# Kernel optimization log

Hardware: AMD Instinct MI355X
Metric: run time of the kernel (lower is better)

The kernel has to match this reference:

```python
import jax, jax.numpy as jnp
import numpy as np

B, CIN, COUT, H, W = 4, 256, 256, 64, 64
EPS = 1e-5


def _conv1x1(x, w, b):
    # x: [B,C,H,W], w: [O,C], b: [O]
    return jnp.einsum('bchw,oc->bohw', x, w) + b[:, None, None]


def _conv3x3(x, w, b):
    y = jax.lax.conv_general_dilated(x, w, (1, 1), 'SAME',
                                     dimension_numbers=('NCHW', 'OIHW', 'NCHW'))
    return y + b[:, None, None]


def _bn(x, g, b, m, v):
    # inference-mode BatchNorm2d
    return g[:, None, None] * (x - m[:, None, None]) * jax.lax.rsqrt(v[:, None, None] + EPS) + b[:, None, None]


def setup_inputs():
    key = jax.random.key(0)
    keys = iter(jax.random.split(key, 64))
    nrm = lambda shape, s=0.05: jax.random.normal(next(keys), shape, dtype=jnp.float32) * s
    uni = lambda shape: jax.random.uniform(next(keys), shape, dtype=jnp.float32, minval=0.5, maxval=1.5)
    C, C2 = COUT, COUT // 2
    d = {}
    d['x'] = nrm((B, CIN, H, W), 1.0)
    d['wq'] = nrm((C2, CIN)); d['bq'] = nrm((C2,))
    d['wk'] = nrm((C2, CIN)); d['bk'] = nrm((C2,))
    d['wv'] = nrm((C, CIN)); d['bv'] = nrm((C,))
    d['d1_w'] = nrm((C, C)); d['d1_b'] = nrm((C,))
    for p in ['bn1', 'lbn1', 'lbn2', 'lbn3']:
        d[p + '_g'] = uni((C,)); d[p + '_b'] = nrm((C,))
        d[p + '_m'] = nrm((C,)); d[p + '_v'] = uni((C,))
    d['l1_w'] = nrm((C, C)); d['l1_b'] = nrm((C,))
    d['l2_w'] = nrm((C, C, 3, 3)); d['l2_b'] = nrm((C,))
    d['l3_w'] = nrm((C, C)); d['l3_b'] = nrm((C,))
    d['r1_w'] = nrm((C2, C)); d['r1_b'] = nrm((C2,))
    d['rbn_g'] = uni((C2,)); d['rbn_b'] = nrm((C2,))
    d['rbn_m'] = nrm((C2,)); d['rbn_v'] = uni((C2,))
    d['r2_w'] = nrm((C, C2)); d['r2_b'] = nrm((C,))
    return d


def _forward(x, wq, bq, wk, bk, wv, bv, d1_w, d1_b,
             bn1_g, bn1_b, bn1_m, bn1_v,
             l1_w, l1_b, lbn1_g, lbn1_b, lbn1_m, lbn1_v,
             l2_w, l2_b, lbn2_g, lbn2_b, lbn2_m, lbn2_v,
             l3_w, l3_b, lbn3_g, lbn3_b, lbn3_m, lbn3_v,
             r1_w, r1_b, rbn_g, rbn_b, rbn_m, rbn_v, r2_w, r2_b):
    b, _, h, w = x.shape
    n = h * w
    q = _conv1x1(x, wq, bq).reshape(b, -1, n)   # [B, C/2, N]
    k = _conv1x1(x, wk, bk).reshape(b, -1, n)   # [B, C/2, N]
    v = _conv1x1(x, wv, bv).reshape(b, -1, n)   # [B, C,   N]
    energy = jnp.einsum('bcn,bcm->bnm', q, k)   # [B, N, N] (query^T key)
    attn = jax.nn.softmax(energy, axis=-1)
    # feature = bmm(value, attn^T): feat[b,c,n] = sum_m v[b,c,m] * attn[b,n,m]
    feat = jnp.einsum('bcm,bnm->bcn', v, attn).reshape(b, -1, h, w)
    # dual1 gate: sigmoid(relu(bn(conv1x1(feat))))
    gate1 = jax.nn.sigmoid(jax.nn.relu(_bn(_conv1x1(feat, d1_w, d1_b), bn1_g, bn1_b, bn1_m, bn1_v)))
    y = feat * gate1
    # dual2_l: 1x1 -> 3x3 -> 1x1 conv/bn/relu stack
    yl = jax.nn.relu(_bn(_conv1x1(y, l1_w, l1_b), lbn1_g, lbn1_b, lbn1_m, lbn1_v))
    yl = jax.nn.relu(_bn(_conv3x3(yl, l2_w, l2_b), lbn2_g, lbn2_b, lbn2_m, lbn2_v))
    yl = jax.nn.relu(_bn(_conv1x1(yl, l3_w, l3_b), lbn3_g, lbn3_b, lbn3_m, lbn3_v))
    # dual2_r: global-avg-pool SE branch
    pooled = jnp.mean(y, axis=(2, 3), keepdims=True)  # [B, C, 1, 1]
    yr = jax.nn.relu(_bn(_conv1x1(pooled, r1_w, r1_b), rbn_g, rbn_b, rbn_m, rbn_v))
    yr = _conv1x1(yr, r2_w, r2_b)
    return feat * jax.nn.sigmoid(yl + yr)


def reference(x, wq, bq, wk, bk, wv, bv, d1_w, d1_b,
              bn1_g, bn1_b, bn1_m, bn1_v,
              l1_w, l1_b, lbn1_g, lbn1_b, lbn1_m, lbn1_v,
              l2_w, l2_b, lbn2_g, lbn2_b, lbn2_m, lbn2_v,
              l3_w, l3_b, lbn3_g, lbn3_b, lbn3_m, lbn3_v,
              r1_w, r1_b, rbn_g, rbn_b, rbn_m, rbn_v, r2_w, r2_b):
    return _forward(x, wq, bq, wk, bk, wv, bv, d1_w, d1_b,
                    bn1_g, bn1_b, bn1_m, bn1_v,
                    l1_w, l1_b, lbn1_g, lbn1_b, lbn1_m, lbn1_v,
                    l2_w, l2_b, lbn2_g, lbn2_b, lbn2_m, lbn2_v,
                    l3_w, l3_b, lbn3_g, lbn3_b, lbn3_m, lbn3_v,
                    r1_w, r1_b, rbn_g, rbn_b, rbn_m, rbn_v, r2_w, r2_b)
```

## Files before the change

kernel.cpp:

```cpp
#include <hip/hip_runtime.h>
#include <math.h>

#define NPIX 4096
#define EPSBN 1e-5f

typedef __attribute__((ext_vector_type(8))) short bf16x8;
typedef __attribute__((ext_vector_type(4))) float f32x4;

__device__ __forceinline__ float sigmoidf_(float x) { return 1.0f / (1.0f + expf(-x)); }

__device__ __forceinline__ short f2bf(float f) {
    unsigned u = __float_as_uint(f);
    u += 0x7fffu + ((u >> 16) & 1u);
    return (short)(u >> 16);
}
__device__ __forceinline__ float bf2f(short s) {
    return __uint_as_float(((unsigned)(unsigned short)s) << 16);
}
__device__ __forceinline__ int pk2(float lo, float hi) {
    return (int)(unsigned short)f2bf(lo) | ((int)(unsigned short)f2bf(hi) << 16);
}

__device__ __forceinline__ void gl_lds16(const short* g, short* l) {
    __builtin_amdgcn_global_load_lds(
        (const __attribute__((address_space(1))) void*)g,
        (__attribute__((address_space(3))) void*)l, 16, 0, 0);
}

template <int EPI, int BM, int BN>
__global__ __launch_bounds__(256) void gbt_k(
    const short* __restrict__ A, int lda,
    const short* __restrict__ B, int ldb,
    void* __restrict__ Cv, void* __restrict__ Cv2, int Ktot,
    const float* __restrict__ bias, const float* __restrict__ bias2,
    const float* __restrict__ bng, const float* __restrict__ bnb,
    const float* __restrict__ bnm, const float* __restrict__ bnv,
    const short* __restrict__ aux, const float* __restrict__ yrp)
{
    constexpr int FI = BM / 32, FJ = BN / 32;
    constexpr int SA = BM / 64, SB = BN / 64;
    __shared__ alignas(16) short lsA[2 * BM * 32];
    __shared__ alignas(16) short lsB[2 * BN * 32];

    const int tid = threadIdx.x;
    const int l = tid & 63;
    const int wv = tid >> 6;
    const int wm = wv >> 1, wn = wv & 1;
    const int m0 = blockIdx.y * BM;
    const int n0 = blockIdx.x * BN;

    const short* arow[2];
    const short* brow[2];
#pragma unroll
    for (int s = 0; s < SA; ++s) {
        int r = wv * (16 * SA) + s * 16 + (l >> 2);
        int sd = (l & 3) ^ ((r >> 1) & 3);
        if (EPI == 5) {
            int g = m0 + r;
            int p = (g >> 12) * 4356 + (((g & 4095) >> 6) + 1) * 66 + ((g & 63) + 1);
            arow[s] = A + (size_t)p * 256 + (sd << 3);
        } else {
            arow[s] = A + (size_t)(m0 + r) * lda + (sd << 3);
        }
    }
#pragma unroll
    for (int s = 0; s < SB; ++s) {
        int r = wv * (16 * SB) + s * 16 + (l >> 2);
        int sd = (l & 3) ^ ((r >> 1) & 3);
        brow[s] = B + (size_t)(n0 + r) * ldb + (sd << 3);
    }

    const int ks = l >> 4;
    const int lc = l & 15;
    int aoff[FI], boff[FJ];
#pragma unroll
    for (int f = 0; f < FI; ++f) {
        int ra = wm * (BM / 2) + f * 16 + lc;
        aoff[f] = ra * 64 + ((ks ^ ((ra >> 1) & 3)) << 4);
    }
#pragma unroll
    for (int f = 0; f < FJ; ++f) {
        int rb = wn * (BN / 2) + f * 16 + lc;
        boff[f] = rb * 64 + ((ks ^ ((rb >> 1) & 3)) << 4);
    }

    auto stage = [&](int d, int k0l) {
        int eA, eB;
        if (EPI == 5) {
            int t = k0l >> 8, ci0 = k0l & 255;
            eA = ((t / 3) * 66 + (t % 3) - 67) * 256 + ci0;
            eB = t * 65536 + ci0;
        } else {
            eA = k0l; eB = k0l;
        }
        short* dA = lsA + d * (BM * 32) + wv * (SA * 512);
        short* dB = lsB + d * (BN * 32) + wv * (SB * 512);
#pragma unroll
        for (int s = 0; s < SA; ++s) gl_lds16(arow[s] + eA, dA + s * 512);
#pragma unroll
        for (int s = 0; s < SB; ++s) gl_lds16(brow[s] + eB, dB + s * 512);
    };

    f32x4 acc[FI][FJ] = {};
    const int nt = Ktot >> 5;

    stage(0, 0);
    __syncthreads();
    int cur = 0;
    for (int t = 0; t < nt; ++t) {
        if (t + 1 < nt) stage(cur ^ 1, (t + 1) << 5);
        bf16x8 af[FI], bfr[FJ];
#pragma unroll
        for (int f = 0; f < FI; ++f)
            af[f] = *(const bf16x8*)((const char*)lsA + cur * (BM * 64) + aoff[f]);
#pragma unroll
        for (int f = 0; f < FJ; ++f)
            bfr[f] = *(const bf16x8*)((const char*)lsB + cur * (BN * 64) + boff[f]);
#pragma unroll
        for (int i = 0; i < FI; ++i)
#pragma unroll
            for (int j = 0; j < FJ; ++j)
                acc[i][j] = __builtin_amdgcn_mfma_f32_16x16x32_bf16(af[i], bfr[j], acc[i][j], 0, 0, 0);
        __syncthreads();
        cur ^= 1;
    }

    const int lr = (l >> 4) << 2;
#pragma unroll
    for (int i = 0; i < FI; ++i) {
        const int rowl = wm * (BM / 2) + i * 16 + lr;
#pragma unroll
        for (int j = 0; j < FJ; ++j) {
            const int coll = n0 + wn * (BN / 2) + j * 16 + lc;

            float sc = 0.f, tc = 0.f, bi = 0.f;
            if constexpr (EPI == 1) {
                bi = (coll < 128) ? bias[coll] : bias2[coll - 128];
            } else if constexpr (EPI == 3 || EPI == 4 || EPI == 5) {
                sc = bng[coll] * rsqrtf(bnv[coll] + EPSBN);
                tc = bnb[coll] - bnm[coll] * sc;
                bi = bias[coll];
            }

#pragma unroll
            for (int r = 0; r < 4; ++r) {
                const int row = m0 + rowl + r;
                float vvv = acc[i][j][r];
                if constexpr (EPI == 1) {
                    float val = vvv + bi;
                    short hi = f2bf(val);
                    short lo = f2bf(val - bf2f(hi));
                    size_t rb = (size_t)row * 256;
                    if (coll < 128) {
                        short* qb_ = (short*)Cv;
                        qb_[rb + coll] = hi;
                        qb_[rb + 128 + coll] = lo;
                    } else {
                        short* kb_ = (short*)Cv2;
                        int c = coll - 128;
                        kb_[rb + c] = hi;
                        kb_[rb + 128 + c] = lo;
                    }
                } else if constexpr (EPI == 2) {
                    int bb = coll >> 12;
                    ((short*)Cv)[((size_t)bb * 256 + row) * 4096 + (coll & 4095)] = f2bf(vvv + bias[row]);
                } else if constexpr (EPI == 3) {
                    float g = sigmoidf_(fmaxf(sc * (vvv + bi) + tc, 0.f));
                    float fv = bf2f(aux[(size_t)row * 256 + coll]);
                    ((short*)Cv)[(size_t)row * 256 + coll] = f2bf(fv * g);
                } else if constexpr (EPI == 4) {
                    float rv = fmaxf(sc * (vvv + bi) + tc, 0.f);
                    int bb = row >> 12, n = row & 4095;
                    int pr = bb * 4356 + ((n >> 6) + 1) * 66 + (n & 63) + 1;
                    ((short*)Cv)[(size_t)pr * 256 + coll] = f2bf(rv);
                } else if constexpr (EPI == 5) {
                    float rv = fmaxf(sc * (vvv + bi) + tc, 0.f);
                    ((short*)Cv)[(size_t)row * 256 + coll] = f2bf(rv);
                } else if constexpr (EPI == 6) {
                    float s6 = bng[row] * rsqrtf(bnv[row] + EPSBN);
                    float t6 = bnb[row] - bnm[row] * s6;
                    int bb = coll >> 12;
                    float yl = fmaxf(s6 * (vvv + bias[row]) + t6, 0.f);
                    float sg = sigmoidf_(yl + yrp[bb * 256 + row]);
                    float fv = bf2f(aux[(size_t)coll * 256 + row]);
                    ((float*)Cv)[((size_t)bb * 256 + row) * 4096 + (coll & 4095)] = fv * sg;
                }
            }
        }
    }
}

__global__ __launch_bounds__(512, 2) void flash_k(
    const short* __restrict__ Q, const short* __restrict__ K,
    const short* __restrict__ V, float* __restrict__ Op, float* __restrict__ lp)
{
    __shared__ alignas(16) short smem[32768];

    const int tid = threadIdx.x;
    const int l = tid & 63;
    const int wv = tid >> 6;
    const int bid = blockIdx.x;
    const int combo = bid & 15;
    const int batch = combo >> 2;
    const int kvq = combo & 3;
    const int q0 = (bid >> 4) * 256;
    const int kv0 = kvq * 1024;

    const short* Qb = Q + (size_t)batch * 4096 * 256;
    const short* Kb = K + (size_t)batch * 4096 * 256;
    const short* Vb = V + (size_t)batch * 256 * 4096;

    const int lc = l & 15, ks = l >> 4;

    bf16x8 bq[2][8];
#pragma unroll
    for (int f = 0; f < 2; ++f)
#pragma unroll
        for (int cc = 0; cc < 8; ++cc)
            bq[f][cc] = *(const bf16x8*)(Qb +
                (size_t)(q0 + wv * 32 + f * 16 + lc) * 256 + cc * 32 + ks * 8);

    const short* ksrc[2]; short* kdst[2];
    const short* vsrc[2]; short* vdst[2];
#pragma unroll
    for (int i = 0; i < 2; ++i) {
        int row = wv * 4 + i * 2 + (l >> 5);
        int s = l & 31;
        int g = s ^ (row & 7);
        ksrc[i] = Kb + (size_t)(kv0 + row) * 256 + g * 8;
        kdst[i] = smem + wv * 1024 + i * 512;
        int c = wv * 32 + i * 16 + (l >> 2);
        int sv = l & 3;
        int gv = sv ^ ((c >> 1) & 3);
        vsrc[i] = Vb + (size_t)c * 4096 + kv0 + gv * 8;
        vdst[i] = smem + 16384 + wv * 1024 + i * 512;
    }
    auto stageKV = [&](int buf, int t) {
#pragma unroll
        for (int i = 0; i < 2; ++i) gl_lds16(ksrc[i] + (size_t)t * 8192, kdst[i] + buf * 8192);
#pragma unroll
        for (int i = 0; i < 2; ++i) gl_lds16(vsrc[i] + t * 32, vdst[i] + buf * 8192);
    };

    stageKV(0, 0);
    __syncthreads();

    const int kro = lc * 512;
    const int kxr = lc & 7;
    const int vb0 = lc * 64 + ((ks ^ ((lc >> 1) & 3)) << 4);
    const int addrA = (((ks & 1) * 2) * 16 + lc) * 4;
    const int addrB = addrA + 64;

    bf16x8 ones;
#pragma unroll
    for (int e = 0; e < 8; ++e) ones[e] = (short)0x3F80;

    f32x4 acc_o[2][16] = {};
    f32x4 acc_l[2] = {};

    int cur = 0;
    for (int t = 0; t < 32; ++t) {
        if (t + 1 < 32) stageKV(cur ^ 1, t + 1);

        const char* kb_ = (const char*)smem + cur * 16384;
        f32x4 s00 = {}, s01 = {}, s10 = {}, s11 = {};
        __builtin_amdgcn_s_setprio(1);
#pragma unroll
        for (int jc = 0; jc < 4; ++jc) {
#pragma unroll
            for (int kvf = 0; kvf < 2; ++kvf) {
                const char* rb_ = kb_ + kro + kvf * 8192;
                bf16x8 kh_ = *(const bf16x8*)(rb_ + ((((jc * 4) + ks) ^ kxr) << 4));
                bf16x8 kl_ = *(const bf16x8*)(rb_ + (((((jc + 4) * 4) + ks) ^ kxr) << 4));
                f32x4& sA = kvf ? s01 : s00;
                f32x4& sB = kvf ? s11 : s10;
                sA = __builtin_amdgcn_mfma_f32_16x16x32_bf16(kh_, bq[0][jc], sA, 0, 0, 0);
                sB = __builtin_amdgcn_mfma_f32_16x16x32_bf16(kh_, bq[1][jc], sB, 0, 0, 0);
                sA = __builtin_amdgcn_mfma_f32_16x16x32_bf16(kl_, bq[0][jc], sA, 0, 0, 0);
                sB = __builtin_amdgcn_mfma_f32_16x16x32_bf16(kl_, bq[1][jc], sB, 0, 0, 0);
                sA = __builtin_amdgcn_mfma_f32_16x16x32_bf16(kh_, bq[0][jc + 4], sA, 0, 0, 0);
                sB = __builtin_amdgcn_mfma_f32_16x16x32_bf16(kh_, bq[1][jc + 4], sB, 0, 0, 0);
            }
        }
        __builtin_amdgcn_s_setprio(0);

        bf16x8 pa[2];
#pragma unroll
        for (int f = 0; f < 2; ++f) {
            const f32x4& sa = f ? s10 : s00;
            const f32x4& sb = f ? s11 : s01;
            int u0 = pk2(__expf(sa[0]), __expf(sa[1]));
            int u1 = pk2(__expf(sa[2]), __expf(sa[3]));
            int u2 = pk2(__expf(sb[0]), __expf(sb[1]));
            int u3 = pk2(__expf(sb[2]), __expf(sb[3]));
            int a0 = __builtin_amdgcn_ds_bpermute(addrA, u0);
            int b0 = __builtin_amdgcn_ds_bpermute(addrA, u2);
            int a1 = __builtin_amdgcn_ds_bpermute(addrA, u1);
            int b1 = __builtin_amdgcn_ds_bpermute(addrA, u3);
            int a2 = __builtin_amdgcn_ds_bpermute(addrB, u0);
            int b2 = __builtin_amdgcn_ds_bpermute(addrB, u2);
            int a3 = __builtin_amdgcn_ds_bpermute(addrB, u1);
            int b3 = __builtin_amdgcn_ds_bpermute(addrB, u3);
            union { int i4[4]; bf16x8 v; } un;
            un.i4[0] = (ks < 2) ? a0 : b0;
            un.i4[1] = (ks < 2) ? a1 : b1;
            un.i4[2] = (ks < 2) ? a2 : b2;
            un.i4[3] = (ks < 2) ? a3 : b3;
            pa[f] = un.v;
        }

        const char* vbb = (const char*)smem + 32768 + cur * 16384;
        __builtin_amdgcn_s_setprio(1);
#pragma unroll
        for (int j = 0; j < 16; ++j) {
            bf16x8 vv = *(const bf16x8*)(vbb + vb0 + j * 1024);
            acc_o[0][j] = __builtin_amdgcn_mfma_f32_16x16x32_bf16(pa[0], vv, acc_o[0][j], 0, 0, 0);
            acc_o[1][j] = __builtin_amdgcn_mfma_f32_16x16x32_bf16(pa[1], vv, acc_o[1][j], 0, 0, 0);
        }
        acc_l[0] = __builtin_amdgcn_mfma_f32_16x16x32_bf16(pa[0], ones, acc_l[0], 0, 0, 0);
        acc_l[1] = __builtin_amdgcn_mfma_f32_16x16x32_bf16(pa[1], ones, acc_l[1], 0, 0, 0);
        __builtin_amdgcn_s_setprio(0);
        __syncthreads();
        cur ^= 1;
    }

    float* Ob = Op + ((size_t)combo * 4096 + q0 + wv * 32) * 256;
#pragma unroll
    for (int f = 0; f < 2; ++f)
#pragma unroll
        for (int j = 0; j < 16; ++j)
#pragma unroll
            for (int r = 0; r < 4; ++r)
                Ob[(size_t)(f * 16 + ks * 4 + r) * 256 + j * 16 + lc] = acc_o[f][j][r];
    if (lc == 0) {
        float* lb = lp + (size_t)combo * 4096 + q0 + wv * 32;
#pragma unroll
        for (int f = 0; f < 2; ++f)
#pragma unroll
            for (int r = 0; r < 4; ++r)
                lb[f * 16 + ks * 4 + r] = acc_l[f][r];
    }
}

__global__ __launch_bounds__(256) void combine_k(const float* __restrict__ Op,
                                                 const float* __restrict__ lp,
                                                 short* __restrict__ o)
{
    int idx = blockIdx.x * 256 + threadIdx.x;
    size_t e = (size_t)idx * 4;
    int row = (int)(e >> 8);
    int batch = row >> 12, ql = row & 4095;
    int c = (int)(e & 255);
    size_t lbase = (size_t)batch * 4 * 4096 + ql;
    float li = 1.0f / (lp[lbase] + lp[lbase + 4096] + lp[lbase + 8192] + lp[lbase + 12288]);
    size_t base = ((size_t)(batch * 4) * 4096 + ql) * 256 + c;
    const float4 a = *(const float4*)(Op + base);
    const float4 b = *(const float4*)(Op + base + 1048576);
    const float4 cc = *(const float4*)(Op + base + 2097152);
    const float4 d = *(const float4*)(Op + base + 3145728);
    short4 o4;
    o4.x = f2bf((a.x + b.x + cc.x + d.x) * li);
    o4.y = f2bf((a.y + b.y + cc.y + d.y) * li);
    o4.z = f2bf((a.z + b.z + cc.z + d.z) * li);
    o4.w = f2bf((a.w + b.w + cc.w + d.w) * li);
    *(short4*)(o + (size_t)row * 256 + c) = o4;
}

__global__ __launch_bounds__(256) void transpose_x_k(const float* __restrict__ x,
                                                     short* __restrict__ xT3)
{
    __shared__ float t[64][65];
    const int b = blockIdx.z, c0 = blockIdx.y * 64, n0 = blockIdx.x * 64;
    const int tid = threadIdx.x;
#pragma unroll
    for (int rep = 0; rep < 16; ++rep) {
        int idx = tid + rep * 256;
        int i = idx >> 6, j = idx & 63;
        t[i][j] = x[((size_t)(b * 256 + c0 + i)) * NPIX + n0 + j];
    }
    __syncthreads();
#pragma unroll
    for (int rep = 0; rep < 16; ++rep) {
        int idx = tid + rep * 256;
        int i = idx >> 6, j = idx & 63;
        float v = t[j][i];
        short hi = f2bf(v);
        short lo = f2bf(v - bf2f(hi));
        size_t rb = ((size_t)(b * NPIX + n0 + i)) * 768;
        xT3[rb + c0 + j] = hi;
        xT3[rb + 256 + c0 + j] = hi;
        xT3[rb + 512 + c0 + j] = lo;
    }
}

__global__ __launch_bounds__(256) void cvt_hilo3_k(const float* __restrict__ src,
                                                   short* __restrict__ dst)
{
    int idx = blockIdx.x * 256 + threadIdx.x;
    int o = idx >> 8, c = idx & 255;
    float v = src[idx];
    short hi = f2bf(v);
    short lo = f2bf(v - bf2f(hi));
    size_t rb = (size_t)o * 768;
    dst[rb + c] = hi;
    dst[rb + 256 + c] = lo;
    dst[rb + 512 + c] = hi;
}

__global__ __launch_bounds__(256) void cvt_k(const float* __restrict__ s,
                                             short* __restrict__ d, int n)
{
    int i = blockIdx.x * 256 + threadIdx.x;
    if (i < n) d[i] = f2bf(s[i]);
}

__global__ __launch_bounds__(256) void permw2_k(const float* __restrict__ l2w,
                                                short* __restrict__ w2)
{
    int idx = blockIdx.x * 256 + threadIdx.x;
    int t = idx >> 16;
    int rem = idx & 65535;
    int co = rem >> 8, ci = rem & 255;
    w2[idx] = f2bf(l2w[((size_t)(co * 256 + ci)) * 9 + t]);
}

__global__ __launch_bounds__(256) void pool_s1_k(const short* __restrict__ yT,
                                                 float* __restrict__ ppart)
{
    const int ns = blockIdx.x, cg = blockIdx.y, b = blockIdx.z;
    const int tid = threadIdx.x;
    const int cl = tid & 63, ph = tid >> 6;
    float s = 0.f;
    const int nbase = ns * 256;
    for (int n = ph; n < 256; n += 4)
        s += bf2f(yT[((size_t)(b * NPIX + nbase + n)) * 256 + cg * 64 + cl]);
    __shared__ float ls[4][64];
    ls[ph][cl] = s;
    __syncthreads();
    if (ph == 0)
        ppart[((size_t)(b * 4 + cg) * 16 + ns) * 64 + cl] =
            ls[0][cl] + ls[1][cl] + ls[2][cl] + ls[3][cl];
}

__global__ __launch_bounds__(256) void pool_s2_k(const float* __restrict__ ppart,
                                                 float* __restrict__ pooled)
{
    const int b = blockIdx.x;
    const int c = threadIdx.x;
    const int cg = c >> 6, cl = c & 63;
    float s = 0.f;
#pragma unroll
    for (int ns = 0; ns < 16; ++ns)
        s += ppart[((size_t)(b * 4 + cg) * 16 + ns) * 64 + cl];
    pooled[b * 256 + c] = s * (1.0f / NPIX);
}

__global__ __launch_bounds__(256) void se_k(
    const float* __restrict__ pooled,
    const float* __restrict__ r1w, const float* __restrict__ r1b,
    const float* __restrict__ g, const float* __restrict__ bb,
    const float* __restrict__ m, const float* __restrict__ vv,
    const float* __restrict__ r2w, const float* __restrict__ r2b,
    float* __restrict__ yr)
{
    const int b = blockIdx.x;
    const int tid = threadIdx.x;
    __shared__ float p[256], hbuf[128];
    p[tid] = pooled[b * 256 + tid];
    __syncthreads();
    if (tid < 128) {
        float a = r1b[tid];
        for (int ci = 0; ci < 256; ++ci) a = fmaf(r1w[tid * 256 + ci], p[ci], a);
        float s = g[tid] * rsqrtf(vv[tid] + EPSBN);
        float t = bb[tid] - m[tid] * s;
        hbuf[tid] = fmaxf(s * a + t, 0.f);
    }
    __syncthreads();
    float a = r2b[tid];
    for (int c2 = 0; c2 < 128; ++c2) a = fmaf(r2w[tid * 128 + c2], hbuf[c2], a);
    yr[b * 256 + tid] = a;
}

extern "C" void kernel_launch(void* const* d_in, const int* in_sizes, int n_in,
                              void* d_out, int out_size, void* d_ws, size_t ws_size,
                              hipStream_t stream)
{
    const float* x    = (const float*)d_in[0];
    const float* wq   = (const float*)d_in[1];
    const float* bq   = (const float*)d_in[2];
    const float* wk   = (const float*)d_in[3];
    const float* bk   = (const float*)d_in[4];
    const float* wvp  = (const float*)d_in[5];
    const float* bv   = (const float*)d_in[6];
    const float* d1w  = (const float*)d_in[7];
    const float* d1b  = (const float*)d_in[8];
    const float* bn1g = (const float*)d_in[9];
    const float* bn1b = (const float*)d_in[10];
    const float* bn1m = (const float*)d_in[11];
    const float* bn1v = (const float*)d_in[12];
    const float* lbn1g = (const float*)d_in[13];
    const float* lbn1b = (const float*)d_in[14];
    const float* lbn1m = (const float*)d_in[15];
    const float* lbn1v = (const float*)d_in[16];
    const float* lbn2g = (const float*)d_in[17];
    const float* lbn2b = (const float*)d_in[18];
    const float* lbn2m = (const float*)d_in[19];
    const float* lbn2v = (const float*)d_in[20];
    const float* lbn3g = (const float*)d_in[21];
    const float* lbn3b = (const float*)d_in[22];
    const float* lbn3m = (const float*)d_in[23];
    const float* lbn3v = (const float*)d_in[24];
    const float* l1w  = (const float*)d_in[25];
    const float* l1b  = (const float*)d_in[26];
    const float* l2w  = (const float*)d_in[27];
    const float* l2b  = (const float*)d_in[28];
    const float* l3w  = (const float*)d_in[29];
    const float* l3b  = (const float*)d_in[30];
    const float* r1w  = (const float*)d_in[31];
    const float* r1b  = (const float*)d_in[32];
    const float* rbng = (const float*)d_in[33];
    const float* rbnb = (const float*)d_in[34];
    const float* rbnm = (const float*)d_in[35];
    const float* rbnv = (const float*)d_in[36];
    const float* r2w  = (const float*)d_in[37];
    const float* r2b  = (const float*)d_in[38];

    float* out = (float*)d_out;
    char* wsb = (char*)d_ws;

    short* xT3  = (short*)(wsb);
    short* qbuf = (short*)(wsb + (24ull << 20));
    short* kbuf = (short*)(wsb + (32ull << 20));
    short* vbuf = (short*)(wsb + (40ull << 20));
    float* Opart= (float*)(wsb + (48ull << 20));
    short* featT= (short*)(wsb + (112ull << 20));
    float* lpart= (float*)(wsb + (120ull << 20));
    short* yT   = (short*)(wsb + (48ull << 20));
    short* t1pad= (short*)(wsb + (56ull << 20));
    short* t2T  = (short*)(wsb + (65ull << 20));
    short* wqk3 = (short*)(wsb + (121ull << 20));
    short* wvb  = wqk3 + 196608;
    short* d1wb = wvb + 65536;
    short* l1wb = d1wb + 65536;
    short* l3wb = l1wb + 65536;
    short* w2b  = l3wb + 65536;
    float* pooled = (float*)(wsb + (123ull << 20) + (512ull << 10));
    float* yrb  = pooled + 1024;
    float* ppart= yrb + 1024;

    dim3 blk(256);

    transpose_x_k<<<dim3(64, 4, 4), blk, 0, stream>>>(x, xT3);
    cvt_hilo3_k<<<128, blk, 0, stream>>>(wq, wqk3);
    cvt_hilo3_k<<<128, blk, 0, stream>>>(wk, wqk3 + (size_t)128 * 768);
    cvt_k<<<256, blk, 0, stream>>>(wvp, wvb, 65536);
    cvt_k<<<256, blk, 0, stream>>>(d1w, d1wb, 65536);
    cvt_k<<<256, blk, 0, stream>>>(l1w, l1wb, 65536);
    cvt_k<<<256, blk, 0, stream>>>(l3w, l3wb, 65536);
    permw2_k<<<2304, blk, 0, stream>>>(l2w, w2b);

    gbt_k<1, 64, 64><<<dim3(4, 256), blk, 0, stream>>>(xT3, 768, wqk3, 768, qbuf, kbuf, 768,
        bq, bk, nullptr, nullptr, nullptr, nullptr, nullptr, nullptr);
    gbt_k<2, 64, 64><<<dim3(256, 4), blk, 0, stream>>>(wvb, 256, xT3, 768, vbuf, nullptr, 256,
        bv, nullptr, nullptr, nullptr, nullptr, nullptr, nullptr, nullptr);

    flash_k<<<256, dim3(512), 0, stream>>>(qbuf, kbuf, vbuf, Opart, lpart);
    combine_k<<<4096, blk, 0, stream>>>(Opart, lpart, featT);

    gbt_k<3, 64, 64><<<dim3(4, 256), blk, 0, stream>>>(featT, 256, d1wb, 256, yT, nullptr, 256,
        d1b, nullptr, bn1g, bn1b, bn1m, bn1v, featT, nullptr);

    hipMemsetAsync(t1pad, 0, (size_t)4 * 4356 * 256 * 2, stream);

    pool_s1_k<<<dim3(16, 4, 4), blk, 0, stream>>>(yT, ppart);
    pool_s2_k<<<4, blk, 0, stream>>>(ppart, pooled);
    se_k<<<4, blk, 0, stream>>>(pooled, r1w, r1b, rbng, rbnb, rbnm, rbnv, r2w, r2b, yrb);

    gbt_k<4, 64, 64><<<dim3(4, 256), blk, 0, stream>>>(yT, 256, l1wb, 256, t1pad, nullptr, 256,
        l1b, nullptr, lbn1g, lbn1b, lbn1m, lbn1v, nullptr, nullptr);
    gbt_k<5, 128, 64><<<dim3(4, 128), blk, 0, stream>>>(t1pad, 256, w2b, 256, t2T, nullptr, 2304,
        l2b, nullptr, lbn2g, lbn2b, lbn2m, lbn2v, nullptr, nullptr);

    gbt_k<6, 64, 64><<<dim3(256, 4), blk, 0, stream>>>(l3wb, 256, t2T, 256, out, nullptr, 256,
        l3b, nullptr, lbn3g, lbn3b, lbn3m, lbn3v, featT, yrb);
}
```

Baseline: 264.5 us.

## Store flash partials as bf16, fuse weight prep kernels, enlarge GEMM tiles

The flash-attention partial outputs are now stored as bf16 instead of fp32, halving the write and read traffic between flash_k and combine_k. That adds rounding before the four split-KV partials are summed. The seven weight-conversion launches are merged into one prep_k kernel to cut launch overhead. Several gbt_k GEMMs switch from 64x64 to 128x64 or 64x128 tiles, giving fewer, larger blocks.

```diff
diff --git a/kernel.cpp b/kernel.cpp
--- a/kernel.cpp
+++ b/kernel.cpp
@@ -192,7 +192,7 @@
 
 __global__ __launch_bounds__(512, 2) void flash_k(
     const short* __restrict__ Q, const short* __restrict__ K,
-    const short* __restrict__ V, float* __restrict__ Op, float* __restrict__ lp)
+    const short* __restrict__ V, short* __restrict__ Op, float* __restrict__ lp)
 {
     __shared__ alignas(16) short smem[32768];
 
@@ -324,14 +324,14 @@
         cur ^= 1;
     }
 
-    float* Ob = Op + ((size_t)combo * 4096 + q0 + wv * 32) * 256;
+    short* Ob = Op + ((size_t)combo * 4096 + q0 + wv * 32) * 256;
 #pragma unroll
     for (int f = 0; f < 2; ++f)
 #pragma unroll
         for (int j = 0; j < 16; ++j)
 #pragma unroll
             for (int r = 0; r < 4; ++r)
-                Ob[(size_t)(f * 16 + ks * 4 + r) * 256 + j * 16 + lc] = acc_o[f][j][r];
+                Ob[(size_t)(f * 16 + ks * 4 + r) * 256 + j * 16 + lc] = f2bf(acc_o[f][j][r]);
     if (lc == 0) {
         float* lb = lp + (size_t)combo * 4096 + q0 + wv * 32;
 #pragma unroll
@@ -342,7 +342,7 @@
     }
 }
 
-__global__ __launch_bounds__(256) void combine_k(const float* __restrict__ Op,
+__global__ __launch_bounds__(256) void combine_k(const short* __restrict__ Op,
                                                  const float* __restrict__ lp,
                                                  short* __restrict__ o)
 {
@@ -354,15 +354,15 @@
     size_t lbase = (size_t)batch * 4 * 4096 + ql;
     float li = 1.0f / (lp[lbase] + lp[lbase + 4096] + lp[lbase + 8192] + lp[lbase + 12288]);
     size_t base = ((size_t)(batch * 4) * 4096 + ql) * 256 + c;
-    const float4 a = *(const float4*)(Op + base);
-    const float4 b = *(const float4*)(Op + base + 1048576);
-    const float4 cc = *(const float4*)(Op + base + 2097152);
-    const float4 d = *(const float4*)(Op + base + 3145728);
+    const short4 a = *(const short4*)(Op + base);
+    const short4 b = *(const short4*)(Op + base + 1048576);
+    const short4 cc = *(const short4*)(Op + base + 2097152);
+    const short4 d = *(const short4*)(Op + base + 3145728);
     short4 o4;
-    o4.x = f2bf((a.x + b.x + cc.x + d.x) * li);
-    o4.y = f2bf((a.y + b.y + cc.y + d.y) * li);
-    o4.z = f2bf((a.z + b.z + cc.z + d.z) * li);
-    o4.w = f2bf((a.w + b.w + cc.w + d.w) * li);
+    o4.x = f2bf((bf2f(a.x) + bf2f(b.x) + bf2f(cc.x) + bf2f(d.x)) * li);
+    o4.y = f2bf((bf2f(a.y) + bf2f(b.y) + bf2f(cc.y) + bf2f(d.y)) * li);
+    o4.z = f2bf((bf2f(a.z) + bf2f(b.z) + bf2f(cc.z) + bf2f(d.z)) * li);
+    o4.w = f2bf((bf2f(a.w) + bf2f(b.w) + bf2f(cc.w) + bf2f(d.w)) * li);
     *(short4*)(o + (size_t)row * 256 + c) = o4;
 }
 
@@ -393,35 +393,40 @@
     }
 }
 
-__global__ __launch_bounds__(256) void cvt_hilo3_k(const float* __restrict__ src,
-                                                   short* __restrict__ dst)
-{
-    int idx = blockIdx.x * 256 + threadIdx.x;
-    int o = idx >> 8, c = idx & 255;
-    float v = src[idx];
-    short hi = f2bf(v);
-    short lo = f2bf(v - bf2f(hi));
-    size_t rb = (size_t)o * 768;
-    dst[rb + c] = hi;
-    dst[rb + 256 + c] = lo;
-    dst[rb + 512 + c] = hi;
-}
-
-__global__ __launch_bounds__(256) void cvt_k(const float* __restrict__ s,
-                                             short* __restrict__ d, int n)
-{
-    int i = blockIdx.x * 256 + threadIdx.x;
-    if (i < n) d[i] = f2bf(s[i]);
-}
-
-__global__ __launch_bounds__(256) void permw2_k(const float* __restrict__ l2w,
-                                                short* __restrict__ w2)
-{
-    int idx = blockIdx.x * 256 + threadIdx.x;
-    int t = idx >> 16;
-    int rem = idx & 65535;
-    int co = rem >> 8, ci = rem & 255;
-    w2[idx] = f2bf(l2w[((size_t)(co * 256 + ci)) * 9 + t]);
+__global__ __launch_bounds__(256) void prep_k(
+    const float* __restrict__ wq, const float* __restrict__ wk,
+    const float* __restrict__ wvp, const float* __restrict__ d1w,
+    const float* __restrict__ l1w, const float* __restrict__ l3w,
+    const float* __restrict__ l2w,
+    short* __restrict__ wqk3, short* __restrict__ wvb, short* __restrict__ d1wb,
+    short* __restrict__ l1wb, short* __restrict__ l3wb, short* __restrict__ w2b)
+{
+    const int b = blockIdx.x;
+    const int tid = threadIdx.x;
+    if (b < 256) {
+        int idx = b * 256 + tid;
+        int o = idx >> 8, c = idx & 255;
+        const float* src = (o < 128) ? wq : wk;
+        float v = src[(o & 127) * 256 + c];
+        short hi = f2bf(v);
+        short lo = f2bf(v - bf2f(hi));
+        size_t rb = (size_t)o * 768;
+        wqk3[rb + c] = hi;
+        wqk3[rb + 256 + c] = lo;
+        wqk3[rb + 512 + c] = hi;
+    } else if (b < 1280) {
+        int g = (b - 256) >> 8;
+        int i = ((b - 256) & 255) * 256 + tid;
+        const float* s = g == 0 ? wvp : g == 1 ? d1w : g == 2 ? l1w : l3w;
+        short* d = g == 0 ? wvb : g == 1 ? d1wb : g == 2 ? l1wb : l3wb;
+        d[i] = f2bf(s[i]);
+    } else {
+        int idx = (b - 1280) * 256 + tid;
+        int t = idx >> 16;
+        int rem = idx & 65535;
+        int co = rem >> 8, ci = rem & 255;
+        w2b[idx] = f2bf(l2w[((size_t)(co * 256 + ci)) * 9 + t]);
+    }
 }
 
 __global__ __launch_bounds__(256) void pool_s1_k(const short* __restrict__ yT,
@@ -532,7 +537,7 @@
     short* qbuf = (short*)(wsb + (24ull << 20));
     short* kbuf = (short*)(wsb + (32ull << 20));
     short* vbuf = (short*)(wsb + (40ull << 20));
-    float* Opart= (float*)(wsb + (48ull << 20));
+    short* Opart= (short*)(wsb + (48ull << 20));
     short* featT= (short*)(wsb + (112ull << 20));
     float* lpart= (float*)(wsb + (120ull << 20));
     short* yT   = (short*)(wsb + (48ull << 20));
@@ -551,23 +556,18 @@
     dim3 blk(256);
 
     transpose_x_k<<<dim3(64, 4, 4), blk, 0, stream>>>(x, xT3);
-    cvt_hilo3_k<<<128, blk, 0, stream>>>(wq, wqk3);
-    cvt_hilo3_k<<<128, blk, 0, stream>>>(wk, wqk3 + (size_t)128 * 768);
-    cvt_k<<<256, blk, 0, stream>>>(wvp, wvb, 65536);
-    cvt_k<<<256, blk, 0, stream>>>(d1w, d1wb, 65536);
-    cvt_k<<<256, blk, 0, stream>>>(l1w, l1wb, 65536);
-    cvt_k<<<256, blk, 0, stream>>>(l3w, l3wb, 65536);
-    permw2_k<<<2304, blk, 0, stream>>>(l2w, w2b);
-
-    gbt_k<1, 64, 64><<<dim3(4, 256), blk, 0, stream>>>(xT3, 768, wqk3, 768, qbuf, kbuf, 768,
+    prep_k<<<3584, blk, 0, stream>>>(wq, wk, wvp, d1w, l1w, l3w, l2w,
+                                     wqk3, wvb, d1wb, l1wb, l3wb, w2b);
+
+    gbt_k<1, 128, 64><<<dim3(4, 128), blk, 0, stream>>>(xT3, 768, wqk3, 768, qbuf, kbuf, 768,
         bq, bk, nullptr, nullptr, nullptr, nullptr, nullptr, nullptr);
-    gbt_k<2, 64, 64><<<dim3(256, 4), blk, 0, stream>>>(wvb, 256, xT3, 768, vbuf, nullptr, 256,
+    gbt_k<2, 64, 128><<<dim3(128, 4), blk, 0, stream>>>(wvb, 256, xT3, 768, vbuf, nullptr, 256,
         bv, nullptr, nullptr, nullptr, nullptr, nullptr, nullptr, nullptr);
 
     flash_k<<<256, dim3(512), 0, stream>>>(qbuf, kbuf, vbuf, Opart, lpart);
     combine_k<<<4096, blk, 0, stream>>>(Opart, lpart, featT);
 
-    gbt_k<3, 64, 64><<<dim3(4, 256), blk, 0, stream>>>(featT, 256, d1wb, 256, yT, nullptr, 256,
+    gbt_k<3, 128, 64><<<dim3(4, 128), blk, 0, stream>>>(featT, 256, d1wb, 256, yT, nullptr, 256,
         d1b, nullptr, bn1g, bn1b, bn1m, bn1v, featT, nullptr);
 
     hipMemsetAsync(t1pad, 0, (size_t)4 * 4356 * 256 * 2, stream);
@@ -576,11 +576,11 @@
     pool_s2_k<<<4, blk, 0, stream>>>(ppart, pooled);
     se_k<<<4, blk, 0, stream>>>(pooled, r1w, r1b, rbng, rbnb, rbnm, rbnv, r2w, r2b, yrb);
 
-    gbt_k<4, 64, 64><<<dim3(4, 256), blk, 0, stream>>>(yT, 256, l1wb, 256, t1pad, nullptr, 256,
+    gbt_k<4, 128, 64><<<dim3(4, 128), blk, 0, stream>>>(yT, 256, l1wb, 256, t1pad, nullptr, 256,
         l1b, nullptr, lbn1g, lbn1b, lbn1m, lbn1v, nullptr, nullptr);
     gbt_k<5, 128, 64><<<dim3(4, 128), blk, 0, stream>>>(t1pad, 256, w2b, 256, t2T, nullptr, 2304,
         l2b, nullptr, lbn2g, lbn2b, lbn2m, lbn2v, nullptr, nullptr);
 
-    gbt_k<6, 64, 64><<<dim3(256, 4), blk, 0, stream>>>(l3wb, 256, t2T, 256, out, nullptr, 256,
+    gbt_k<6, 64, 128><<<dim3(128, 4), blk, 0, stream>>>(l3wb, 256, t2T, 256, out, nullptr, 256,
         l3b, nullptr, lbn3g, lbn3b, lbn3m, lbn3v, featT, yrb);
 }
```

Result: faster. 250.5 us (-5.3%).
